# Optimization experiments

Measured on AMD Instinct MI355X. Metric: run time of the kernel, lower is better.

The kernel has to match this reference:

```python
import jax, jax.numpy as jnp
import numpy as np

N_NODES = 50000


def setup_inputs() -> dict:
    key = jax.random.key(0)
    k1, k2, k3, k4 = jax.random.split(key, 4)
    in_f, out_f = 128, 128
    n_edges = 625000
    x = jax.random.normal(k1, (N_NODES, in_f), dtype=jnp.float32)
    index = jax.random.randint(k2, (2, n_edges), 0, N_NODES, dtype=jnp.int64)
    # reset_parameters uses uniform(-1/sqrt(in), 1/sqrt(in))
    bound = 1.0 / np.sqrt(in_f)
    weight = jax.random.uniform(k3, (in_f, out_f), minval=-bound, maxval=bound, dtype=jnp.float32)
    bias = jax.random.uniform(k4, (out_f,), minval=-bound, maxval=bound, dtype=jnp.float32)
    return {"x": x, "index": index, "weight": weight, "bias": bias}


def reference(x, index, weight, bias):
    # F_out = D_hat^{-1/2} (A + I) D_hat^{-1/2} X W + b
    n = x.shape[0]
    loops = jnp.arange(n, dtype=index.dtype)
    src = jnp.concatenate([index[0], loops])  # [E + N]
    dst = jnp.concatenate([index[1], loops])
    # degrees of A_hat (counted on destination nodes)
    deg = jax.ops.segment_sum(jnp.ones_like(dst, dtype=x.dtype), dst, num_segments=n)
    dinv = jax.lax.rsqrt(jnp.maximum(deg, 1e-12))
    norm = dinv[src] * dinv[dst]  # [E + N]
    h = x @ weight  # [N, out] dense GEMM first (out <= in)
    msg = h[src] * norm[:, None]  # gather + scale
    out = jax.ops.segment_sum(msg, dst, num_segments=n)  # scatter-add
    return out + bias
```

## Files before the change

### kernel.cpp

```cpp
#include <hip/hip_runtime.h>

#define F     128
#define PAD   64
#define CHUNK 2048

typedef short short8 __attribute__((ext_vector_type(8)));
typedef float f32x4v __attribute__((ext_vector_type(4)));

__device__ __forceinline__ ushort f2bf(float f) {
    uint b = __float_as_uint(f);
    uint r = (b + 0x7fffu + ((b >> 16) & 1u)) >> 16;
    return (ushort)r;
}
__device__ __forceinline__ float bflo(uint v) { return __uint_as_float(v << 16); }
__device__ __forceinline__ float bfhi(uint v) { return __uint_as_float(v & 0xffff0000u); }


__global__ __launch_bounds__(256) void prep(
    const float* __restrict__ w, ushort* __restrict__ wt,
    int* __restrict__ cnt, int n)
{
    int i = blockIdx.x * 256 + threadIdx.x;
    if (i < n) cnt[i] = 0;
    if (blockIdx.x == 0) {
        for (int idx = threadIdx.x; idx < F * 32; idx += 256) {
            int k = idx >> 5, c4 = idx & 31;
            float4 v = *reinterpret_cast<const float4*>(&w[k * F + c4 * 4]);
            wt[(c4 * 4 + 0) * F + k] = f2bf(v.x);
            wt[(c4 * 4 + 1) * F + k] = f2bf(v.y);
            wt[(c4 * 4 + 2) * F + k] = f2bf(v.z);
            wt[(c4 * 4 + 3) * F + k] = f2bf(v.w);
        }
    }
}


__global__ __launch_bounds__(256) void hybrid(
    const int* __restrict__ src, const int* __restrict__ dst, int ne,
    int* __restrict__ cnt, ushort* __restrict__ padded, int nbB,
    const float* __restrict__ x, const ushort* __restrict__ wt,
    ushort* __restrict__ g, int n)
{
    if (blockIdx.x < nbB) {
        const int grp = blockIdx.x >> 3;
        const int xcd = blockIdx.x & 7;
        const int sh  = (n + 7) >> 3;
        const int dlo = xcd * sh;
        const int dhi = (dlo + sh) < n ? (dlo + sh) : n;
        const int base = grp * CHUNK;
        const int lim  = (base + CHUNK) < ne ? (base + CHUNK) : ne;
        for (int e0 = base + threadIdx.x * 4; e0 < lim; e0 += 1024) {
            if (e0 + 3 < lim) {
                int4 s4 = *reinterpret_cast<const int4*>(&src[e0]);
                int4 d4 = *reinterpret_cast<const int4*>(&dst[e0]);
                if (d4.x >= dlo && d4.x < dhi) {
                    int p = atomicAdd(&cnt[d4.x], 1);
                    if (p < PAD) padded[(size_t)d4.x * PAD + p] = (ushort)s4.x;
                }
                if (d4.y >= dlo && d4.y < dhi) {
                    int p = atomicAdd(&cnt[d4.y], 1);
                    if (p < PAD) padded[(size_t)d4.y * PAD + p] = (ushort)s4.y;
                }
                if (d4.z >= dlo && d4.z < dhi) {
                    int p = atomicAdd(&cnt[d4.z], 1);
                    if (p < PAD) padded[(size_t)d4.z * PAD + p] = (ushort)s4.z;
                }
                if (d4.w >= dlo && d4.w < dhi) {
                    int p = atomicAdd(&cnt[d4.w], 1);
                    if (p < PAD) padded[(size_t)d4.w * PAD + p] = (ushort)s4.w;
                }
            } else {
                for (int e = e0; e < lim; ++e) {
                    int d = dst[e];
                    if (d >= dlo && d < dhi) {
                        int p = atomicAdd(&cnt[d], 1);
                        if (p < PAD) padded[(size_t)d * PAD + p] = (ushort)src[e];
                    }
                }
            }
        }
        return;
    }

    const int gb   = blockIdx.x - nbB;
    const int t    = threadIdx.x;
    const int lane = t & 63;
    const int wv   = t >> 6;
    const int wr   = wv >> 1, wc = wv & 1;
    const int l15  = lane & 15, kg = lane >> 4;
    const int row0 = gb * 64 + wr * 32;
    const int col0 = wc * 64;

    f32x4v acc[2][4];
    #pragma unroll
    for (int rt = 0; rt < 2; ++rt)
        #pragma unroll
        for (int ct = 0; ct < 4; ++ct)
            acc[rt][ct] = (f32x4v){0.f, 0.f, 0.f, 0.f};

    #pragma unroll
    for (int kt = 0; kt < 4; ++kt) {
        const int k0 = kt * 32 + kg * 8;
        short8 a[2];
        #pragma unroll
        for (int rt = 0; rt < 2; ++rt) {
            int row = row0 + rt * 16 + l15;
            row = row < n ? row : n - 1;
            float4 p0 = *reinterpret_cast<const float4*>(&x[(size_t)row * F + k0]);
            float4 p1 = *reinterpret_cast<const float4*>(&x[(size_t)row * F + k0 + 4]);
            ushort u[8] = {f2bf(p0.x), f2bf(p0.y), f2bf(p0.z), f2bf(p0.w),
                           f2bf(p1.x), f2bf(p1.y), f2bf(p1.z), f2bf(p1.w)};
            a[rt] = *reinterpret_cast<short8*>(u);
        }
        short8 b[4];
        #pragma unroll
        for (int ct = 0; ct < 4; ++ct) {
            int col = col0 + ct * 16 + l15;
            b[ct] = *reinterpret_cast<const short8*>(&wt[col * F + k0]);
        }
        #pragma unroll
        for (int rt = 0; rt < 2; ++rt)
            #pragma unroll
            for (int ct = 0; ct < 4; ++ct)
                acc[rt][ct] = __builtin_amdgcn_mfma_f32_16x16x32_bf16(
                    a[rt], b[ct], acc[rt][ct], 0, 0, 0);
    }

    #pragma unroll
    for (int rt = 0; rt < 2; ++rt) {
        int rbase = row0 + rt * 16 + kg * 4;
        #pragma unroll
        for (int ct = 0; ct < 4; ++ct) {
            int col = col0 + ct * 16 + l15;
            #pragma unroll
            for (int rr = 0; rr < 4; ++rr) {
                int row = rbase + rr;
                if (row < n)
                    g[(size_t)row * F + col] = f2bf(acc[rt][ct][rr]);
            }
        }
    }
}


__global__ __launch_bounds__(256) void gather_bf16(
    const int* __restrict__ cnt, const ushort* __restrict__ padded,
    const ushort* __restrict__ g, const float* __restrict__ bias,
    float* __restrict__ out, int n)
{
    int wid  = (blockIdx.x * 256 + threadIdx.x) >> 6;
    int lane = threadIdx.x & 63;
    if (wid >= n) return;
    wid = __builtin_amdgcn_readfirstlane(wid);
    const int c = lane * 2;

    int   cv = cnt[wid];
    float dv = rsqrtf((float)cv + 1.0f);
    uint self = *reinterpret_cast<const uint*>(&g[(size_t)wid * F + c]);
    float ax = dv * bflo(self), ay = dv * bfhi(self);

    int m = cv < PAD ? cv : PAD;
    const ushort* pl = padded + (size_t)wid * PAD;

    int j = 0;
    for (; j + 4 <= m; j += 4) {
        int s0 = pl[j + 0], s1 = pl[j + 1], s2 = pl[j + 2], s3 = pl[j + 3];
        float d0 = rsqrtf((float)cnt[s0] + 1.0f);
        float d1 = rsqrtf((float)cnt[s1] + 1.0f);
        float d2 = rsqrtf((float)cnt[s2] + 1.0f);
        float d3 = rsqrtf((float)cnt[s3] + 1.0f);
        uint v0 = *reinterpret_cast<const uint*>(&g[(size_t)s0 * F + c]);
        uint v1 = *reinterpret_cast<const uint*>(&g[(size_t)s1 * F + c]);
        uint v2 = *reinterpret_cast<const uint*>(&g[(size_t)s2 * F + c]);
        uint v3 = *reinterpret_cast<const uint*>(&g[(size_t)s3 * F + c]);
        ax = fmaf(d0, bflo(v0), ax); ay = fmaf(d0, bfhi(v0), ay);
        ax = fmaf(d1, bflo(v1), ax); ay = fmaf(d1, bfhi(v1), ay);
        ax = fmaf(d2, bflo(v2), ax); ay = fmaf(d2, bfhi(v2), ay);
        ax = fmaf(d3, bflo(v3), ax); ay = fmaf(d3, bfhi(v3), ay);
    }
    for (; j < m; ++j) {
        int s = pl[j];
        float ds = rsqrtf((float)cnt[s] + 1.0f);
        uint v = *reinterpret_cast<const uint*>(&g[(size_t)s * F + c]);
        ax = fmaf(ds, bflo(v), ax);
        ay = fmaf(ds, bfhi(v), ay);
    }

    float2 bb = *reinterpret_cast<const float2*>(&bias[c]);
    float2 o;
    o.x = fmaf(dv, ax, bb.x);
    o.y = fmaf(dv, ay, bb.y);
    *reinterpret_cast<float2*>(&out[(size_t)wid * F + c]) = o;
}


__global__ __launch_bounds__(256) void gemm_scale(
    const float* __restrict__ x, const float* __restrict__ w,
    const float* __restrict__ dinv, float* __restrict__ g, int n)
{
    __shared__ float sWl[F * F];
    __shared__ float sXl[8][F];
    for (int i = threadIdx.x; i < F * F; i += 256) sWl[i] = w[i];
    __syncthreads();
    const int r  = threadIdx.x >> 5;
    const int cg = threadIdx.x & 31;
    for (int row0 = blockIdx.x * 8; row0 < n; row0 += gridDim.x * 8) {
        {
            int t4 = threadIdx.x * 4;
            int rr = t4 >> 7, cc = t4 & (F - 1);
            if (row0 + rr < n) {
                float4 v = *reinterpret_cast<const float4*>(&x[(size_t)(row0 + rr) * F + cc]);
                *reinterpret_cast<float4*>(&sXl[rr][cc]) = v;
            }
        }
        __syncthreads();
        int row = row0 + r;
        if (row < n) {
            float4 acc = make_float4(0.f, 0.f, 0.f, 0.f);
            const float* xr = sXl[r];
            #pragma unroll 8
            for (int k = 0; k < F; ++k) {
                float  xv = xr[k];
                float4 wv = *reinterpret_cast<const float4*>(&sWl[k * F + cg * 4]);
                acc.x = fmaf(xv, wv.x, acc.x);
                acc.y = fmaf(xv, wv.y, acc.y);
                acc.z = fmaf(xv, wv.z, acc.z);
                acc.w = fmaf(xv, wv.w, acc.w);
            }
            float s = dinv[row];
            acc.x *= s; acc.y *= s; acc.z *= s; acc.w *= s;
            *reinterpret_cast<float4*>(&g[(size_t)row * F + cg * 4]) = acc;
        }
        __syncthreads();
    }
}

__global__ void init_degf(float* __restrict__ deg, int n) {
    int i = blockIdx.x * blockDim.x + threadIdx.x;
    if (i < n) deg[i] = 1.0f;
}
__global__ void count_degf(const int* __restrict__ dst, int ne, float* __restrict__ deg) {
    int e = blockIdx.x * blockDim.x + threadIdx.x;
    if (e < ne) atomicAdd(&deg[dst[e]], 1.0f);
}
__global__ void calc_dinvf(const float* __restrict__ deg, float* __restrict__ dinv, int n) {
    int i = blockIdx.x * blockDim.x + threadIdx.x;
    if (i < n) dinv[i] = rsqrtf(fmaxf(deg[i], 1e-12f));
}
__global__ __launch_bounds__(256) void scatter_edges(
    const int* __restrict__ src, const int* __restrict__ dst, int ne,
    const float* __restrict__ g, float* __restrict__ out)
{
    int gid  = (blockIdx.x * blockDim.x + threadIdx.x) >> 5;
    int lane = threadIdx.x & 31;
    if (gid >= ne) return;
    int s = src[gid], d = dst[gid];
    float4 v = *reinterpret_cast<const float4*>(&g[(size_t)s * F + lane * 4]);
    float* op = &out[(size_t)d * F + lane * 4];
    atomicAdd(op + 0, v.x);
    atomicAdd(op + 1, v.y);
    atomicAdd(op + 2, v.z);
    atomicAdd(op + 3, v.w);
}
__global__ __launch_bounds__(256) void finalize(
    float* __restrict__ out, const float* __restrict__ g,
    const float* __restrict__ dinv, const float* __restrict__ bias, int n)
{
    int i = blockIdx.x * blockDim.x + threadIdx.x;
    if (i >= n * 32) return;
    int row = i >> 5, c4 = i & 31;
    float  s = dinv[row];
    float4 o = *reinterpret_cast<float4*>(&out[(size_t)i * 4]);
    float4 gg = *reinterpret_cast<const float4*>(&g[(size_t)i * 4]);
    float4 b = *reinterpret_cast<const float4*>(&bias[c4 * 4]);
    o.x = fmaf(s, o.x + gg.x, b.x);
    o.y = fmaf(s, o.y + gg.y, b.y);
    o.z = fmaf(s, o.z + gg.z, b.z);
    o.w = fmaf(s, o.w + gg.w, b.w);
    *reinterpret_cast<float4*>(&out[(size_t)i * 4]) = o;
}


extern "C" void kernel_launch(void* const* d_in, const int* in_sizes, int n_in,
                              void* d_out, int out_size, void* d_ws, size_t ws_size,
                              hipStream_t stream) {
    const float* x     = (const float*)d_in[0];
    const int*   index = (const int*)d_in[1];
    const float* w     = (const float*)d_in[2];
    const float* bias  = (const float*)d_in[3];
    float*       out   = (float*)d_out;

    int n  = in_sizes[0] / F;
    int ne = in_sizes[1] / 2;
    const int* src = index;
    const int* dst = index + ne;

    size_t b_cnt    = 0;
    size_t b_wt     = (b_cnt + (size_t)n * 4 + 15) & ~(size_t)15;
    size_t b_padded = (b_wt + (size_t)F * F * 2 + 15) & ~(size_t)15;
    size_t b_g      = (b_padded + (size_t)n * PAD * 2 + 15) & ~(size_t)15;
    size_t need     = b_g + (size_t)n * F * 2;

    char* wsb = (char*)d_ws;
    int*    cnt    = (int*)(wsb + b_cnt);
    ushort* wt     = (ushort*)(wsb + b_wt);
    ushort* padded = (ushort*)(wsb + b_padded);
    ushort* g      = (ushort*)(wsb + b_g);

    int nb  = (n + 255) / 256;
    int nbB = ((ne + CHUNK - 1) / CHUNK) * 8;
    int nbG = (n + 63) / 64;

    if (ws_size >= need && n <= 65535) {
        prep<<<nb, 256, 0, stream>>>(w, wt, cnt, n);
        hybrid<<<nbB + nbG, 256, 0, stream>>>(src, dst, ne, cnt, padded, nbB, x, wt, g, n);
        int gb = (int)(((long long)n * 64 + 255) / 256);
        gather_bf16<<<gb, 256, 0, stream>>>(cnt, padded, g, bias, out, n);
    } else {
        float* degf  = (float*)wsb;
        float* dinvf = (float*)wsb + n;
        float* gf    = (float*)wsb + 2 * n;
        int nbE = (ne + 255) / 256;
        hipMemsetAsync(d_out, 0, (size_t)out_size * sizeof(float), stream);
        init_degf<<<nb, 256, 0, stream>>>(degf, n);
        count_degf<<<nbE, 256, 0, stream>>>(dst, ne, degf);
        calc_dinvf<<<nb, 256, 0, stream>>>(degf, dinvf, n);
        gemm_scale<<<(n + 7) / 8, 256, 0, stream>>>(x, w, dinvf, gf, n);
        int sc_blocks = (int)(((long long)ne * 32 + 255) / 256);
        scatter_edges<<<sc_blocks, 256, 0, stream>>>(src, dst, ne, gf, out);
        finalize<<<(n * 32 + 255) / 256, 256, 0, stream>>>(out, gf, dinvf, bias, n);
    }
}
```

Measured before the change: 105.6 us.

## Drop prep kernel, read fp32 weights directly, simplify edge bucketing

Removes the prep kernel that zeroed counters and transposed the weights to bf16. Counters are now cleared with hipMemsetAsync, and the GEMM blocks convert the fp32 weight column on the fly using strided scalar loads. The XCD-partitioned chunked edge bucketing is replaced by one edge per thread, which gives up the locality of atomics per XCD. The intent is to save a launch and transpose pass, at the cost of uncoalesced weight loads and more scattered atomics.

```diff
diff --git a/kernel.cpp b/kernel.cpp
--- a/kernel.cpp
+++ b/kernel.cpp
@@ -1,8 +1,7 @@
 #include <hip/hip_runtime.h>
 
-#define F     128
-#define PAD   64
-#define CHUNK 2048
+#define F   128
+#define PAD 64
 
 typedef short short8 __attribute__((ext_vector_type(8)));
 typedef float f32x4v __attribute__((ext_vector_type(4)));
@@ -16,68 +15,18 @@
 __device__ __forceinline__ float bfhi(uint v) { return __uint_as_float(v & 0xffff0000u); }
 
 
-__global__ __launch_bounds__(256) void prep(
-    const float* __restrict__ w, ushort* __restrict__ wt,
-    int* __restrict__ cnt, int n)
-{
-    int i = blockIdx.x * 256 + threadIdx.x;
-    if (i < n) cnt[i] = 0;
-    if (blockIdx.x == 0) {
-        for (int idx = threadIdx.x; idx < F * 32; idx += 256) {
-            int k = idx >> 5, c4 = idx & 31;
-            float4 v = *reinterpret_cast<const float4*>(&w[k * F + c4 * 4]);
-            wt[(c4 * 4 + 0) * F + k] = f2bf(v.x);
-            wt[(c4 * 4 + 1) * F + k] = f2bf(v.y);
-            wt[(c4 * 4 + 2) * F + k] = f2bf(v.z);
-            wt[(c4 * 4 + 3) * F + k] = f2bf(v.w);
-        }
-    }
-}
-
-
 __global__ __launch_bounds__(256) void hybrid(
     const int* __restrict__ src, const int* __restrict__ dst, int ne,
     int* __restrict__ cnt, ushort* __restrict__ padded, int nbB,
-    const float* __restrict__ x, const ushort* __restrict__ wt,
+    const float* __restrict__ x, const float* __restrict__ w,
     ushort* __restrict__ g, int n)
 {
     if (blockIdx.x < nbB) {
-        const int grp = blockIdx.x >> 3;
-        const int xcd = blockIdx.x & 7;
-        const int sh  = (n + 7) >> 3;
-        const int dlo = xcd * sh;
-        const int dhi = (dlo + sh) < n ? (dlo + sh) : n;
-        const int base = grp * CHUNK;
-        const int lim  = (base + CHUNK) < ne ? (base + CHUNK) : ne;
-        for (int e0 = base + threadIdx.x * 4; e0 < lim; e0 += 1024) {
-            if (e0 + 3 < lim) {
-                int4 s4 = *reinterpret_cast<const int4*>(&src[e0]);
-                int4 d4 = *reinterpret_cast<const int4*>(&dst[e0]);
-                if (d4.x >= dlo && d4.x < dhi) {
-                    int p = atomicAdd(&cnt[d4.x], 1);
-                    if (p < PAD) padded[(size_t)d4.x * PAD + p] = (ushort)s4.x;
-                }
-                if (d4.y >= dlo && d4.y < dhi) {
-                    int p = atomicAdd(&cnt[d4.y], 1);
-                    if (p < PAD) padded[(size_t)d4.y * PAD + p] = (ushort)s4.y;
-                }
-                if (d4.z >= dlo && d4.z < dhi) {
-                    int p = atomicAdd(&cnt[d4.z], 1);
-                    if (p < PAD) padded[(size_t)d4.z * PAD + p] = (ushort)s4.z;
-                }
-                if (d4.w >= dlo && d4.w < dhi) {
-                    int p = atomicAdd(&cnt[d4.w], 1);
-                    if (p < PAD) padded[(size_t)d4.w * PAD + p] = (ushort)s4.w;
-                }
-            } else {
-                for (int e = e0; e < lim; ++e) {
-                    int d = dst[e];
-                    if (d >= dlo && d < dhi) {
-                        int p = atomicAdd(&cnt[d], 1);
-                        if (p < PAD) padded[(size_t)d * PAD + p] = (ushort)src[e];
-                    }
-                }
-            }
+        int e = blockIdx.x * 256 + threadIdx.x;
+        if (e < ne) {
+            int s = src[e], d = dst[e];
+            int p = atomicAdd(&cnt[d], 1);
+            if (p < PAD) padded[(size_t)d * PAD + p] = (ushort)s;
         }
         return;
     }
@@ -116,7 +65,11 @@
         #pragma unroll
         for (int ct = 0; ct < 4; ++ct) {
             int col = col0 + ct * 16 + l15;
-            b[ct] = *reinterpret_cast<const short8*>(&wt[col * F + k0]);
+            ushort u[8];
+            #pragma unroll
+            for (int j = 0; j < 8; ++j)
+                u[j] = f2bf(w[(size_t)(k0 + j) * F + col]);
+            b[ct] = *reinterpret_cast<short8*>(u);
         }
         #pragma unroll
         for (int rt = 0; rt < 2; ++rt)
@@ -296,30 +249,28 @@
     const int* dst = index + ne;
 
     size_t b_cnt    = 0;
-    size_t b_wt     = (b_cnt + (size_t)n * 4 + 15) & ~(size_t)15;
-    size_t b_padded = (b_wt + (size_t)F * F * 2 + 15) & ~(size_t)15;
+    size_t b_padded = (b_cnt + (size_t)n * 4 + 15) & ~(size_t)15;
     size_t b_g      = (b_padded + (size_t)n * PAD * 2 + 15) & ~(size_t)15;
     size_t need     = b_g + (size_t)n * F * 2;
 
     char* wsb = (char*)d_ws;
     int*    cnt    = (int*)(wsb + b_cnt);
-    ushort* wt     = (ushort*)(wsb + b_wt);
     ushort* padded = (ushort*)(wsb + b_padded);
     ushort* g      = (ushort*)(wsb + b_g);
 
-    int nb  = (n + 255) / 256;
-    int nbB = ((ne + CHUNK - 1) / CHUNK) * 8;
+    int nbB = (ne + 255) / 256;
     int nbG = (n + 63) / 64;
 
     if (ws_size >= need && n <= 65535) {
-        prep<<<nb, 256, 0, stream>>>(w, wt, cnt, n);
-        hybrid<<<nbB + nbG, 256, 0, stream>>>(src, dst, ne, cnt, padded, nbB, x, wt, g, n);
+        hipMemsetAsync(cnt, 0, (size_t)n * 4, stream);
+        hybrid<<<nbB + nbG, 256, 0, stream>>>(src, dst, ne, cnt, padded, nbB, x, w, g, n);
         int gb = (int)(((long long)n * 64 + 255) / 256);
         gather_bf16<<<gb, 256, 0, stream>>>(cnt, padded, g, bias, out, n);
     } else {
         float* degf  = (float*)wsb;
         float* dinvf = (float*)wsb + n;
         float* gf    = (float*)wsb + 2 * n;
+        int nb  = (n + 255) / 256;
         int nbE = (ne + 255) / 256;
         hipMemsetAsync(d_out, 0, (size_t)out_size * sizeof(float), stream);
         init_degf<<<nb, 256, 0, stream>>>(degf, n);
```

After: 100.0 us. 5.3% less time.

## Split hybrid bucket/GEMM kernel into separate launches and drop weight prep kernel

Applied to the files above, without the earlier changes.

Replaces the single fused launch, where edge-bucketing blocks and GEMM blocks ran side by side, with a memset, a dedicated bucket kernel using a fixed 1024-block grid and larger per-block edge chunks, and a separate GEMM kernel. The GEMM now converts fp32 weights to bf16 on the fly with strided scalar loads instead of reading a pre-transposed bf16 copy, which removes the prep kernel. This trims launch overhead and per-block work imbalance in bucketing, but gives up the overlap between bucketing and GEMM and adds uncoalesced weight reads inside the GEMM.

```diff
diff --git a/kernel.cpp b/kernel.cpp
--- a/kernel.cpp
+++ b/kernel.cpp
@@ -1,8 +1,8 @@
 #include <hip/hip_runtime.h>
 
-#define F     128
-#define PAD   64
-#define CHUNK 2048
+#define F    128
+#define PAD  64
+#define BKB  1024
 
 typedef short short8 __attribute__((ext_vector_type(8)));
 typedef float f32x4v __attribute__((ext_vector_type(4)));
@@ -16,79 +16,63 @@
 __device__ __forceinline__ float bfhi(uint v) { return __uint_as_float(v & 0xffff0000u); }
 
 
-__global__ __launch_bounds__(256) void prep(
-    const float* __restrict__ w, ushort* __restrict__ wt,
-    int* __restrict__ cnt, int n)
-{
-    int i = blockIdx.x * 256 + threadIdx.x;
-    if (i < n) cnt[i] = 0;
-    if (blockIdx.x == 0) {
-        for (int idx = threadIdx.x; idx < F * 32; idx += 256) {
-            int k = idx >> 5, c4 = idx & 31;
-            float4 v = *reinterpret_cast<const float4*>(&w[k * F + c4 * 4]);
-            wt[(c4 * 4 + 0) * F + k] = f2bf(v.x);
-            wt[(c4 * 4 + 1) * F + k] = f2bf(v.y);
-            wt[(c4 * 4 + 2) * F + k] = f2bf(v.z);
-            wt[(c4 * 4 + 3) * F + k] = f2bf(v.w);
-        }
-    }
-}
-
-
-__global__ __launch_bounds__(256) void hybrid(
+__global__ __launch_bounds__(256) void bucket(
     const int* __restrict__ src, const int* __restrict__ dst, int ne,
-    int* __restrict__ cnt, ushort* __restrict__ padded, int nbB,
-    const float* __restrict__ x, const ushort* __restrict__ wt,
+    int* __restrict__ cnt, ushort* __restrict__ padded, int n)
+{
+    const int xcd   = blockIdx.x & 7;
+    const int slice = blockIdx.x >> 3;
+    const int nsl   = BKB >> 3;
+    int chunk = ((ne + nsl - 1) / nsl + 3) & ~3;
+    const int sh  = (n + 7) >> 3;
+    const int dlo = xcd * sh;
+    const int dhi = (dlo + sh) < n ? (dlo + sh) : n;
+    const int base = slice * chunk;
+    const int lim  = (base + chunk) < ne ? (base + chunk) : ne;
+
+    for (int e0 = base + threadIdx.x * 4; e0 < lim; e0 += 1024) {
+        if (e0 + 3 < lim) {
+            int4 s4 = *reinterpret_cast<const int4*>(&src[e0]);
+            int4 d4 = *reinterpret_cast<const int4*>(&dst[e0]);
+            if (d4.x >= dlo && d4.x < dhi) {
+                int p = atomicAdd(&cnt[d4.x], 1);
+                if (p < PAD) padded[(size_t)d4.x * PAD + p] = (ushort)s4.x;
+            }
+            if (d4.y >= dlo && d4.y < dhi) {
+                int p = atomicAdd(&cnt[d4.y], 1);
+                if (p < PAD) padded[(size_t)d4.y * PAD + p] = (ushort)s4.y;
+            }
+            if (d4.z >= dlo && d4.z < dhi) {
+                int p = atomicAdd(&cnt[d4.z], 1);
+                if (p < PAD) padded[(size_t)d4.z * PAD + p] = (ushort)s4.z;
+            }
+            if (d4.w >= dlo && d4.w < dhi) {
+                int p = atomicAdd(&cnt[d4.w], 1);
+                if (p < PAD) padded[(size_t)d4.w * PAD + p] = (ushort)s4.w;
+            }
+        } else {
+            for (int e = e0; e < lim; ++e) {
+                int d = dst[e];
+                if (d >= dlo && d < dhi) {
+                    int p = atomicAdd(&cnt[d], 1);
+                    if (p < PAD) padded[(size_t)d * PAD + p] = (ushort)src[e];
+                }
+            }
+        }
+    }
+}
+
+
+__global__ __launch_bounds__(256) void gemm(
+    const float* __restrict__ x, const float* __restrict__ w,
     ushort* __restrict__ g, int n)
 {
-    if (blockIdx.x < nbB) {
-        const int grp = blockIdx.x >> 3;
-        const int xcd = blockIdx.x & 7;
-        const int sh  = (n + 7) >> 3;
-        const int dlo = xcd * sh;
-        const int dhi = (dlo + sh) < n ? (dlo + sh) : n;
-        const int base = grp * CHUNK;
-        const int lim  = (base + CHUNK) < ne ? (base + CHUNK) : ne;
-        for (int e0 = base + threadIdx.x * 4; e0 < lim; e0 += 1024) {
-            if (e0 + 3 < lim) {
-                int4 s4 = *reinterpret_cast<const int4*>(&src[e0]);
-                int4 d4 = *reinterpret_cast<const int4*>(&dst[e0]);
-                if (d4.x >= dlo && d4.x < dhi) {
-                    int p = atomicAdd(&cnt[d4.x], 1);
-                    if (p < PAD) padded[(size_t)d4.x * PAD + p] = (ushort)s4.x;
-                }
-                if (d4.y >= dlo && d4.y < dhi) {
-                    int p = atomicAdd(&cnt[d4.y], 1);
-                    if (p < PAD) padded[(size_t)d4.y * PAD + p] = (ushort)s4.y;
-                }
-                if (d4.z >= dlo && d4.z < dhi) {
-                    int p = atomicAdd(&cnt[d4.z], 1);
-                    if (p < PAD) padded[(size_t)d4.z * PAD + p] = (ushort)s4.z;
-                }
-                if (d4.w >= dlo && d4.w < dhi) {
-                    int p = atomicAdd(&cnt[d4.w], 1);
-                    if (p < PAD) padded[(size_t)d4.w * PAD + p] = (ushort)s4.w;
-                }
-            } else {
-                for (int e = e0; e < lim; ++e) {
-                    int d = dst[e];
-                    if (d >= dlo && d < dhi) {
-                        int p = atomicAdd(&cnt[d], 1);
-                        if (p < PAD) padded[(size_t)d * PAD + p] = (ushort)src[e];
-                    }
-                }
-            }
-        }
-        return;
-    }
-
-    const int gb   = blockIdx.x - nbB;
     const int t    = threadIdx.x;
     const int lane = t & 63;
     const int wv   = t >> 6;
     const int wr   = wv >> 1, wc = wv & 1;
     const int l15  = lane & 15, kg = lane >> 4;
-    const int row0 = gb * 64 + wr * 32;
+    const int row0 = blockIdx.x * 64 + wr * 32;
     const int col0 = wc * 64;
 
     f32x4v acc[2][4];
@@ -116,7 +100,11 @@
         #pragma unroll
         for (int ct = 0; ct < 4; ++ct) {
             int col = col0 + ct * 16 + l15;
-            b[ct] = *reinterpret_cast<const short8*>(&wt[col * F + k0]);
+            ushort u[8];
+            #pragma unroll
+            for (int j = 0; j < 8; ++j)
+                u[j] = f2bf(w[(size_t)(k0 + j) * F + col]);
+            b[ct] = *reinterpret_cast<short8*>(u);
         }
         #pragma unroll
         for (int rt = 0; rt < 2; ++rt)
@@ -296,30 +284,28 @@
     const int* dst = index + ne;
 
     size_t b_cnt    = 0;
-    size_t b_wt     = (b_cnt + (size_t)n * 4 + 15) & ~(size_t)15;
-    size_t b_padded = (b_wt + (size_t)F * F * 2 + 15) & ~(size_t)15;
+    size_t b_padded = (b_cnt + (size_t)n * 4 + 15) & ~(size_t)15;
     size_t b_g      = (b_padded + (size_t)n * PAD * 2 + 15) & ~(size_t)15;
     size_t need     = b_g + (size_t)n * F * 2;
 
     char* wsb = (char*)d_ws;
     int*    cnt    = (int*)(wsb + b_cnt);
-    ushort* wt     = (ushort*)(wsb + b_wt);
     ushort* padded = (ushort*)(wsb + b_padded);
     ushort* g      = (ushort*)(wsb + b_g);
 
-    int nb  = (n + 255) / 256;
-    int nbB = ((ne + CHUNK - 1) / CHUNK) * 8;
     int nbG = (n + 63) / 64;
 
     if (ws_size >= need && n <= 65535) {
-        prep<<<nb, 256, 0, stream>>>(w, wt, cnt, n);
-        hybrid<<<nbB + nbG, 256, 0, stream>>>(src, dst, ne, cnt, padded, nbB, x, wt, g, n);
+        hipMemsetAsync(cnt, 0, (size_t)n * 4, stream);
+        bucket<<<BKB, 256, 0, stream>>>(src, dst, ne, cnt, padded, n);
+        gemm<<<nbG, 256, 0, stream>>>(x, w, g, n);
         int gb = (int)(((long long)n * 64 + 255) / 256);
         gather_bf16<<<gb, 256, 0, stream>>>(cnt, padded, g, bias, out, n);
     } else {
         float* degf  = (float*)wsb;
         float* dinvf = (float*)wsb + n;
         float* gf    = (float*)wsb + 2 * n;
+        int nb  = (n + 255) / 256;
         int nbE = (ne + 255) / 256;
         hipMemsetAsync(d_out, 0, (size_t)out_size * sizeof(float), stream);
         init_degf<<<nb, 256, 0, stream>>>(degf, n);
```

After: 95.13 us. 9.9% less time.
